# Performance work log

Hardware: AMD Instinct MI355X
Metric: run time of the kernel (lower is better)

## Reference

```python
import jax, jax.numpy as jnp
import numpy as np

B, N, IN_F, OUT_F = 8, 2048, 256, 256
ALPHA = 0.2  # LeakyReLU negative slope
NEG_INF = -1e9


def setup_inputs() -> dict:
    key = jax.random.key(0)
    ks = jax.random.split(key, 8)
    h = jax.random.normal(ks[0], (B, N, IN_F), dtype=jnp.float32)
    adj = jax.random.randint(ks[1], (B, N, N), 0, 2, dtype=jnp.int32)
    # xavier-ish scaled params
    W_w = jax.random.normal(ks[2], (OUT_F, IN_F), dtype=jnp.float32) * (1.414 / np.sqrt(IN_F + OUT_F))
    W_b = jnp.zeros((OUT_F,), dtype=jnp.float32)
    ai_w = jax.random.normal(ks[3], (1, OUT_F), dtype=jnp.float32) * (1.414 / np.sqrt(OUT_F + 1))
    ai_b = jnp.zeros((1,), dtype=jnp.float32)
    aj_w = jax.random.normal(ks[4], (1, OUT_F), dtype=jnp.float32) * (1.414 / np.sqrt(OUT_F + 1))
    aj_b = jnp.zeros((1,), dtype=jnp.float32)
    return {"h": h, "adj": adj, "W_w": W_w, "W_b": W_b,
            "ai_w": ai_w, "ai_b": ai_b, "aj_w": aj_w, "aj_b": aj_b}


def reference(h, adj, W_w, W_b, ai_w, ai_b, aj_w, aj_b):
    # Wh: [B, N, F]
    Wh = jnp.einsum('bni,oi->bno', h, W_w) + W_b
    # additive attention scores (pos_embed_dim == 1 so the .view is a transpose)
    Wh1 = jnp.einsum('bnf,of->bno', Wh, ai_w) + ai_b        # [B, N, 1]
    Wh2 = jnp.einsum('bnf,of->bno', Wh, aj_w) + aj_b        # [B, N, 1]
    e = Wh1 + jnp.swapaxes(Wh2, 1, 2)                       # [B, N, N]
    e = jnp.where(e >= 0, e, ALPHA * e)                     # LeakyReLU
    attention = jnp.where(adj > 0, e, NEG_INF)
    attention = jax.nn.softmax(attention, axis=2)
    # dropout: inference mode (training=False) -> identity
    h_hat = jnp.einsum('bnm,bmf->bnf', attention, Wh)
    return jax.nn.elu(h_hat)  # concat=True
```

## Files before the change

### kernel.cpp

```cpp
#include <hip/hip_runtime.h>

typedef __bf16 bf16;
typedef _Float16 f16;
typedef __bf16 bf16x8 __attribute__((ext_vector_type(8)));
typedef _Float16 f16x8 __attribute__((ext_vector_type(8)));
typedef float  f32x4  __attribute__((ext_vector_type(4)));

#define B_  8
#define N_  2048
#define F_  256
#define NTOK (B_ * N_)
#define NH   (NTOK * F_)
#define NW   (F_ * F_)
static constexpr float LOG2E = 1.44269504088896f;

__device__ __forceinline__ int detect_bf16(const void* h) {
    const unsigned* hw = (const unsigned*)h;
    unsigned w = hw[threadIdx.x & 63];
    unsigned ex = (w >> 7) & 0xFFu;
    unsigned long long b = __ballot(ex > 100u && ex < 150u);
    return __popcll(b) >= 40;
}

__device__ __forceinline__ float ldf(const void* p, int i, int isb) {
    return isb ? (float)((const bf16*)p)[i] : ((const float*)p)[i];
}

__device__ __forceinline__ size_t wht2_idx(int b, int f, int n) {
    int jc = n >> 6;
    int slot = ((n >> 3) & 7) ^ (f & 7);
    return (((size_t)(b * 32 + jc) * F_ + f) << 6) + (slot << 3) + (n & 7);
}

__global__ __launch_bounds__(256)
void k_cvt(const void* __restrict__ hv, const void* __restrict__ Wv,
           bf16* __restrict__ hb, bf16* __restrict__ Wb) {
    if (detect_bf16(hv)) return;
    size_t base = ((size_t)blockIdx.x * 256 + threadIdx.x) * 8;
    {
        const float* src = (const float*)hv + base;
        float4 a = *(const float4*)src;
        float4 b = *(const float4*)(src + 4);
        bf16x8 r;
        r[0]=(bf16)a.x; r[1]=(bf16)a.y; r[2]=(bf16)a.z; r[3]=(bf16)a.w;
        r[4]=(bf16)b.x; r[5]=(bf16)b.y; r[6]=(bf16)b.z; r[7]=(bf16)b.w;
        *(bf16x8*)(hb + base) = r;
    }
    if (base < NW) {
        const float* src = (const float*)Wv + base;
        float4 a = *(const float4*)src;
        float4 b = *(const float4*)(src + 4);
        bf16x8 r;
        r[0]=(bf16)a.x; r[1]=(bf16)a.y; r[2]=(bf16)a.z; r[3]=(bf16)a.w;
        r[4]=(bf16)b.x; r[5]=(bf16)b.y; r[6]=(bf16)b.z; r[7]=(bf16)b.w;
        *(bf16x8*)(Wb + base) = r;
    }
}

__global__ __launch_bounds__(256)
void k_wht(const void* __restrict__ hv, const void* __restrict__ Wv,
           const bf16* __restrict__ hcv, const bf16* __restrict__ Wcv,
           const void* __restrict__ Wbv, const void* __restrict__ ai_wv,
           const void* __restrict__ ai_bv, const void* __restrict__ aj_wv,
           const void* __restrict__ aj_bv, bf16* __restrict__ WhT2,
           unsigned* __restrict__ adjw) {
    int isb = detect_bf16(hv);
    const bf16* hb = isb ? (const bf16*)hv : hcv;
    const bf16* Wb = isb ? (const bf16*)Wv : Wcv;
    int ttile = blockIdx.x;
    int fg = threadIdx.x >> 6;
    int lane = threadIdx.x & 63;
    int T0 = ttile * 16;
    int m = lane & 15, quad = lane >> 4;

    f32x4 acc[4];
#pragma unroll
    for (int ft = 0; ft < 4; ++ft) acc[ft] = (f32x4){0.f, 0.f, 0.f, 0.f};

    const bf16* hp = hb + (size_t)(T0 + m) * F_ + quad * 8;
    const bf16* wp = Wb + (size_t)(fg * 64 + m) * F_ + quad * 8;
#pragma unroll
    for (int kk = 0; kk < F_; kk += 32) {
        bf16x8 hf = *(const bf16x8*)(hp + kk);
#pragma unroll
        for (int ft = 0; ft < 4; ++ft) {
            bf16x8 wf = *(const bf16x8*)(wp + (size_t)ft * 16 * F_ + kk);
            acc[ft] = __builtin_amdgcn_mfma_f32_16x16x32_bf16(wf, hf, acc[ft], 0, 0, 0);
        }
    }
    int token = T0 + m;
    int b = token >> 11, n = token & (N_ - 1);
    float s_p = 0.f, t_p = 0.f;
#pragma unroll
    for (int ft = 0; ft < 4; ++ft)
#pragma unroll
        for (int r = 0; r < 4; ++r) {
            int f = fg * 64 + ft * 16 + quad * 4 + r;
            float v = acc[ft][r] + ldf(Wbv, f, isb);
            bf16 vb = (bf16)v;
            WhT2[wht2_idx(b, f, n)] = vb;
            float vr = (float)vb;
            s_p += vr * ldf(ai_wv, f, isb);
            t_p += vr * ldf(aj_wv, f, isb);
        }
    s_p += __shfl_down(s_p, 32, 64); s_p += __shfl_down(s_p, 16, 64);
    t_p += __shfl_down(t_p, 32, 64); t_p += __shfl_down(t_p, 16, 64);
    __shared__ float sred[4][16], tred[4][16];
    if (lane < 16) { sred[fg][lane] = s_p; tred[fg][lane] = t_p; }
    __syncthreads();
    if (threadIdx.x < 16) {
        int tid = threadIdx.x;
        int tok = T0 + tid;
        float ss = (sred[0][tid] + sred[1][tid] + sred[2][tid] + sred[3][tid]
                    + ldf(ai_bv, 0, isb)) * LOG2E;
        float tt = (tred[0][tid] + tred[1][tid] + tred[2][tid] + tred[3][tid]
                    + ldf(aj_bv, 0, isb)) * LOG2E;
        f16 th = (f16)tt, sh = (f16)ss;
        unsigned short tu, su;
        __builtin_memcpy(&tu, &th, 2);
        __builtin_memcpy(&su, &sh, 2);
        unsigned w0 = adjw[tok];
        adjw[tok] = (w0 & 0xFFFFu) | ((unsigned)tu << 16);
        unsigned w1 = adjw[NTOK + tok];
        adjw[NTOK + tok] = (w1 & 0xFFFFu) | ((unsigned)su << 16);
    }
}

__device__ __forceinline__ unsigned char pbits(uint4 a, uint4 b) {
    return (unsigned char)((a.x & 1u) | ((a.y & 1u) << 1) | ((a.z & 1u) << 2) |
                           ((a.w & 1u) << 3) | ((b.x & 1u) << 4) |
                           ((b.y & 1u) << 5) | ((b.z & 1u) << 6) |
                           ((b.w & 1u) << 7));
}

__device__ __forceinline__ void stageB(const bf16* tile, char* dst,
                                       int w, int lane) {
#pragma unroll
    for (int r = 0; r < 8; ++r) {
        int off = (w * 8 + r) * 1024;
        const bf16* g = tile + off / 2 + lane * 8;
        __builtin_amdgcn_global_load_lds(
            (const __attribute__((address_space(1))) unsigned*)g,
            (__attribute__((address_space(3))) unsigned*)(dst + off),
            16, 0, 0);
    }
}

__global__ __launch_bounds__(256)
void k_attn(const unsigned* __restrict__ adjw, const bf16* __restrict__ WhT2,
            const void* __restrict__ hv, void* __restrict__ outv) {
    int isb = detect_bf16(hv);
    int bid = blockIdx.x;
    int b = bid & 7, itile = bid >> 3, i0 = itile * 32;
    int tid = threadIdx.x;
    int w = tid >> 6, lane = tid & 63, m = lane & 15, q = lane >> 4;
    int mt = w >> 1, jh = w & 1;

    __shared__ __align__(16) char smem[70656];
    char* Bbuf0 = smem;
    char* Bbuf1 = smem + 32768;
    f16* tLDS   = (f16*)(smem + 65536);
    unsigned char* pack0 = (unsigned char*)(smem + 69632);
    unsigned char* pack1 = (unsigned char*)(smem + 69888);
    float* red  = (float*)smem;

    const bf16* batch_tiles = WhT2 + ((size_t)b * 32) * F_ * 64;

#pragma unroll
    for (int k = 0; k < 8; ++k) {
        int idx = k * 256 + tid;
        unsigned wv = adjw[b * N_ + idx];
        unsigned short us = (unsigned short)(wv >> 16);
        f16 tv; __builtin_memcpy(&tv, &us, 2);
        tLDS[idx] = tv;
    }
    int row = i0 + mt * 16 + m;
    unsigned swd = adjw[NTOK + b * N_ + row];
    unsigned short su = (unsigned short)(swd >> 16);
    f16 sh; __builtin_memcpy(&sh, &su, 2);
    float s2i = (float)sh;

    int prow = tid >> 3, ps = tid & 7;
    const unsigned* arow = adjw + ((size_t)(b * N_ + i0 + prow)) * N_ + ps * 8;
    {
        uint4 x0 = *(const uint4*)arow, x1 = *(const uint4*)(arow + 4);
        pack0[prow * 8 + ps] = pbits(x0, x1);
    }
    stageB(batch_tiles, Bbuf0, w, lane);
    __syncthreads();

    bf16x8 ones;
#pragma unroll
    for (int k = 0; k < 8; ++k) ones[k] = (bf16)1.0f;

    f32x4 acc[16];
#pragma unroll
    for (int ft = 0; ft < 16; ++ft) acc[ft] = (f32x4){0.f, 0.f, 0.f, 0.f};
    f32x4 acc_l = {0.f, 0.f, 0.f, 0.f};

    for (int c = 0; c < 32; ++c) {
        char* Bcur = (c & 1) ? Bbuf1 : Bbuf0;
        unsigned char* pcur = (c & 1) ? pack1 : pack0;
        uint4 aw0, aw1;
        bool pre = (c < 31);
        if (pre) {
            stageB(batch_tiles + (size_t)(c + 1) * F_ * 64,
                   (c & 1) ? Bbuf0 : Bbuf1, w, lane);
            aw0 = *(const uint4*)(arow + (size_t)(c + 1) * 64);
            aw1 = *(const uint4*)(arow + (size_t)(c + 1) * 64 + 4);
        }
        unsigned long long pb64 =
            *(const unsigned long long*)(pcur + (mt * 16 + m) * 8);
        unsigned bits8 = (unsigned)(pb64 >> ((jh * 4 + q) * 8)) & 0xFFu;
        f16x8 tv = *(const f16x8*)(tLDS + c * 64 + jh * 32 + q * 8);

        bf16x8 af;
#pragma unroll
        for (int qq = 0; qq < 8; ++qq) {
            float x = s2i + (float)tv[qq];
            x = fmaxf(x, 0.2f * x);
            float pv = ((bits8 >> qq) & 1u) ? __builtin_amdgcn_exp2f(x) : 0.f;
            af[qq] = (bf16)pv;
        }
        int sbase = (jh * 4 + q);
#pragma unroll
        for (int ft = 0; ft < 16; ++ft) {
            int fr = ft * 16 + m;
            int psl = sbase ^ (m & 7);
            bf16x8 bfr = *(const bf16x8*)(Bcur + fr * 128 + psl * 16);
            acc[ft] = __builtin_amdgcn_mfma_f32_16x16x32_bf16(af, bfr, acc[ft], 0, 0, 0);
        }
        acc_l = __builtin_amdgcn_mfma_f32_16x16x32_bf16(af, ones, acc_l, 0, 0, 0);
        if (pre)
            ((c & 1) ? pack0 : pack1)[prow * 8 + ps] = pbits(aw0, aw1);
        __syncthreads();
    }

    if (jh == 1) {
#pragma unroll
        for (int r = 0; r < 4; ++r) {
            int rr = mt * 16 + q * 4 + r;
#pragma unroll
            for (int ft = 0; ft < 16; ++ft)
                red[rr * 257 + ft * 16 + m] = acc[ft][r];
            if (m == 0) red[rr * 257 + 256] = acc_l[r];
        }
    }
    __syncthreads();
    if (jh == 0) {
#pragma unroll
        for (int r = 0; r < 4; ++r) {
            int rr = mt * 16 + q * 4 + r;
            float lf = acc_l[r] + red[rr * 257 + 256];
            float rl = (lf > 0.f) ? (1.f / lf) : 0.f;
            size_t ob = ((size_t)b * N_ + i0 + rr) * F_;
#pragma unroll
            for (int ft = 0; ft < 16; ++ft) {
                int f = ft * 16 + m;
                float v = acc[ft][r] + red[rr * 257 + f];
                v *= rl;
                v = (v > 0.f) ? v : (__builtin_amdgcn_exp2f(v * LOG2E) - 1.f);
                if (isb) ((bf16*)outv)[ob + f] = (bf16)v;
                else     ((float*)outv)[ob + f] = v;
            }
        }
    }
}

extern "C" void kernel_launch(void* const* d_in, const int* in_sizes, int n_in,
                              void* d_out, int out_size, void* d_ws, size_t ws_size,
                              hipStream_t stream) {
    (void)in_sizes; (void)n_in; (void)out_size; (void)ws_size;
    const void* h    = d_in[0];
    unsigned*   adjw = (unsigned*)d_in[1];
    const void* W_w  = d_in[2];
    const void* W_b  = d_in[3];
    const void* ai_w = d_in[4];
    const void* ai_b = d_in[5];
    const void* aj_w = d_in[6];
    const void* aj_b = d_in[7];

    bf16* WhT2 = (bf16*)d_ws;
    bf16* hcv  = (bf16*)((char*)d_ws + (8  << 20));
    bf16* Wcv  = (bf16*)((char*)d_ws + (16 << 20));

    k_cvt <<<dim3(2048), dim3(256), 0, stream>>>(h, W_w, hcv, Wcv);
    k_wht <<<dim3(1024), dim3(256), 0, stream>>>(h, W_w, hcv, Wcv, W_b,
                                                 ai_w, ai_b, aj_w, aj_b,
                                                 WhT2, adjw);
    k_attn<<<dim3(512),  dim3(256), 0, stream>>>(adjw, WhT2, h, d_out);
}
```

Before: 262.4 us.

## Double attention row tile per block to reuse staged Wh fragments

Each block of the attention kernel now handles 64 query rows instead of 32. Each wave computes two 16-row MFMA tiles that share the same B-fragment LDS reads and the same staged Wh tiles. The grid is halved to 256 blocks and launch bounds are set to one block per CU, which allows larger accumulator register use. This cuts global and LDS traffic for Wh per output row. In exchange, fewer waves are resident per CU, so there is less latency hiding.

```diff
diff --git a/kernel.cpp b/kernel.cpp
--- a/kernel.cpp
+++ b/kernel.cpp
@@ -10,7 +10,6 @@
 #define N_  2048
 #define F_  256
 #define NTOK (B_ * N_)
-#define NH   (NTOK * F_)
 #define NW   (F_ * F_)
 static constexpr float LOG2E = 1.44269504088896f;
 
@@ -146,22 +145,22 @@
     }
 }
 
-__global__ __launch_bounds__(256)
+__global__ __launch_bounds__(256, 1)
 void k_attn(const unsigned* __restrict__ adjw, const bf16* __restrict__ WhT2,
             const void* __restrict__ hv, void* __restrict__ outv) {
     int isb = detect_bf16(hv);
     int bid = blockIdx.x;
-    int b = bid & 7, itile = bid >> 3, i0 = itile * 32;
+    int b = bid & 7, itile = bid >> 3, i0 = itile * 64;
     int tid = threadIdx.x;
     int w = tid >> 6, lane = tid & 63, m = lane & 15, q = lane >> 4;
-    int mt = w >> 1, jh = w & 1;
+    int mtq = w >> 1, jh = w & 1;
 
     __shared__ __align__(16) char smem[70656];
     char* Bbuf0 = smem;
     char* Bbuf1 = smem + 32768;
     f16* tLDS   = (f16*)(smem + 65536);
     unsigned char* pack0 = (unsigned char*)(smem + 69632);
-    unsigned char* pack1 = (unsigned char*)(smem + 69888);
+    unsigned char* pack1 = (unsigned char*)(smem + 70144);
     float* red  = (float*)smem;
 
     const bf16* batch_tiles = WhT2 + ((size_t)b * 32) * F_ * 64;
@@ -174,17 +173,25 @@
         f16 tv; __builtin_memcpy(&tv, &us, 2);
         tLDS[idx] = tv;
     }
-    int row = i0 + mt * 16 + m;
-    unsigned swd = adjw[NTOK + b * N_ + row];
-    unsigned short su = (unsigned short)(swd >> 16);
-    f16 sh; __builtin_memcpy(&sh, &su, 2);
-    float s2i = (float)sh;
-
-    int prow = tid >> 3, ps = tid & 7;
-    const unsigned* arow = adjw + ((size_t)(b * N_ + i0 + prow)) * N_ + ps * 8;
+    int row0 = i0 + mtq * 32 + m;
+    float s2i0, s2i1;
     {
-        uint4 x0 = *(const uint4*)arow, x1 = *(const uint4*)(arow + 4);
-        pack0[prow * 8 + ps] = pbits(x0, x1);
+        unsigned sw0 = adjw[NTOK + b * N_ + row0];
+        unsigned sw1 = adjw[NTOK + b * N_ + row0 + 16];
+        unsigned short u0 = (unsigned short)(sw0 >> 16);
+        unsigned short u1 = (unsigned short)(sw1 >> 16);
+        f16 h0, h1;
+        __builtin_memcpy(&h0, &u0, 2); __builtin_memcpy(&h1, &u1, 2);
+        s2i0 = (float)h0; s2i1 = (float)h1;
+    }
+
+    int pr = tid >> 2, pp = tid & 3;
+    const unsigned* arow = adjw + ((size_t)(b * N_ + i0 + pr)) * N_ + pp * 16;
+    {
+        uint4 x0 = *(const uint4*)arow,        x1 = *(const uint4*)(arow + 4);
+        uint4 x2 = *(const uint4*)(arow + 8),  x3 = *(const uint4*)(arow + 12);
+        pack0[pr * 8 + pp * 2]     = pbits(x0, x1);
+        pack0[pr * 8 + pp * 2 + 1] = pbits(x2, x3);
     }
     stageB(batch_tiles, Bbuf0, w, lane);
     __syncthreads();
@@ -193,34 +200,47 @@
 #pragma unroll
     for (int k = 0; k < 8; ++k) ones[k] = (bf16)1.0f;
 
-    f32x4 acc[16];
-#pragma unroll
-    for (int ft = 0; ft < 16; ++ft) acc[ft] = (f32x4){0.f, 0.f, 0.f, 0.f};
-    f32x4 acc_l = {0.f, 0.f, 0.f, 0.f};
+    f32x4 acc0[16], acc1[16];
+#pragma unroll
+    for (int ft = 0; ft < 16; ++ft) {
+        acc0[ft] = (f32x4){0.f, 0.f, 0.f, 0.f};
+        acc1[ft] = (f32x4){0.f, 0.f, 0.f, 0.f};
+    }
+    f32x4 acc_l0 = {0.f, 0.f, 0.f, 0.f};
+    f32x4 acc_l1 = {0.f, 0.f, 0.f, 0.f};
 
     for (int c = 0; c < 32; ++c) {
         char* Bcur = (c & 1) ? Bbuf1 : Bbuf0;
         unsigned char* pcur = (c & 1) ? pack1 : pack0;
-        uint4 aw0, aw1;
+        uint4 aw0, aw1, aw2, aw3;
         bool pre = (c < 31);
         if (pre) {
             stageB(batch_tiles + (size_t)(c + 1) * F_ * 64,
                    (c & 1) ? Bbuf0 : Bbuf1, w, lane);
-            aw0 = *(const uint4*)(arow + (size_t)(c + 1) * 64);
-            aw1 = *(const uint4*)(arow + (size_t)(c + 1) * 64 + 4);
-        }
-        unsigned long long pb64 =
-            *(const unsigned long long*)(pcur + (mt * 16 + m) * 8);
-        unsigned bits8 = (unsigned)(pb64 >> ((jh * 4 + q) * 8)) & 0xFFu;
+            const unsigned* ap = arow + (size_t)(c + 1) * 64;
+            aw0 = *(const uint4*)ap;       aw1 = *(const uint4*)(ap + 4);
+            aw2 = *(const uint4*)(ap + 8); aw3 = *(const uint4*)(ap + 12);
+        }
+        unsigned long long pb0 =
+            *(const unsigned long long*)(pcur + (mtq * 32 + m) * 8);
+        unsigned long long pb1 =
+            *(const unsigned long long*)(pcur + (mtq * 32 + 16 + m) * 8);
+        int sh8 = (jh * 4 + q) * 8;
+        unsigned bits0 = (unsigned)(pb0 >> sh8) & 0xFFu;
+        unsigned bits1 = (unsigned)(pb1 >> sh8) & 0xFFu;
         f16x8 tv = *(const f16x8*)(tLDS + c * 64 + jh * 32 + q * 8);
 
-        bf16x8 af;
+        bf16x8 af0, af1;
 #pragma unroll
         for (int qq = 0; qq < 8; ++qq) {
-            float x = s2i + (float)tv[qq];
-            x = fmaxf(x, 0.2f * x);
-            float pv = ((bits8 >> qq) & 1u) ? __builtin_amdgcn_exp2f(x) : 0.f;
-            af[qq] = (bf16)pv;
+            float tq = (float)tv[qq];
+            float x0 = s2i0 + tq, x1 = s2i1 + tq;
+            x0 = fmaxf(x0, 0.2f * x0);
+            x1 = fmaxf(x1, 0.2f * x1);
+            float p0 = ((bits0 >> qq) & 1u) ? __builtin_amdgcn_exp2f(x0) : 0.f;
+            float p1 = ((bits1 >> qq) & 1u) ? __builtin_amdgcn_exp2f(x1) : 0.f;
+            af0[qq] = (bf16)p0;
+            af1[qq] = (bf16)p1;
         }
         int sbase = (jh * 4 + q);
 #pragma unroll
@@ -228,36 +248,65 @@
             int fr = ft * 16 + m;
             int psl = sbase ^ (m & 7);
             bf16x8 bfr = *(const bf16x8*)(Bcur + fr * 128 + psl * 16);
-            acc[ft] = __builtin_amdgcn_mfma_f32_16x16x32_bf16(af, bfr, acc[ft], 0, 0, 0);
-        }
-        acc_l = __builtin_amdgcn_mfma_f32_16x16x32_bf16(af, ones, acc_l, 0, 0, 0);
-        if (pre)
-            ((c & 1) ? pack0 : pack1)[prow * 8 + ps] = pbits(aw0, aw1);
+            acc0[ft] = __builtin_amdgcn_mfma_f32_16x16x32_bf16(af0, bfr, acc0[ft], 0, 0, 0);
+            acc1[ft] = __builtin_amdgcn_mfma_f32_16x16x32_bf16(af1, bfr, acc1[ft], 0, 0, 0);
+        }
+        acc_l0 = __builtin_amdgcn_mfma_f32_16x16x32_bf16(af0, ones, acc_l0, 0, 0, 0);
+        acc_l1 = __builtin_amdgcn_mfma_f32_16x16x32_bf16(af1, ones, acc_l1, 0, 0, 0);
+        if (pre) {
+            unsigned char* pnxt = (c & 1) ? pack0 : pack1;
+            pnxt[pr * 8 + pp * 2]     = pbits(aw0, aw1);
+            pnxt[pr * 8 + pp * 2 + 1] = pbits(aw2, aw3);
+        }
         __syncthreads();
     }
 
     if (jh == 1) {
 #pragma unroll
         for (int r = 0; r < 4; ++r) {
-            int rr = mt * 16 + q * 4 + r;
+            int rr = mtq * 32 + q * 4 + r;
 #pragma unroll
             for (int ft = 0; ft < 16; ++ft)
-                red[rr * 257 + ft * 16 + m] = acc[ft][r];
-            if (m == 0) red[rr * 257 + 256] = acc_l[r];
+                red[rr * 257 + ft * 16 + m] = acc0[ft][r];
+            if (m == 0) red[rr * 257 + 256] = acc_l0[r];
+        }
+#pragma unroll
+        for (int r = 0; r < 4; ++r) {
+            int rr = mtq * 32 + 16 + q * 4 + r;
+#pragma unroll
+            for (int ft = 0; ft < 16; ++ft)
+                red[rr * 257 + ft * 16 + m] = acc1[ft][r];
+            if (m == 0) red[rr * 257 + 256] = acc_l1[r];
         }
     }
     __syncthreads();
     if (jh == 0) {
 #pragma unroll
         for (int r = 0; r < 4; ++r) {
-            int rr = mt * 16 + q * 4 + r;
-            float lf = acc_l[r] + red[rr * 257 + 256];
+            int rr = mtq * 32 + q * 4 + r;
+            float lf = acc_l0[r] + red[rr * 257 + 256];
             float rl = (lf > 0.f) ? (1.f / lf) : 0.f;
             size_t ob = ((size_t)b * N_ + i0 + rr) * F_;
 #pragma unroll
             for (int ft = 0; ft < 16; ++ft) {
                 int f = ft * 16 + m;
-                float v = acc[ft][r] + red[rr * 257 + f];
+                float v = acc0[ft][r] + red[rr * 257 + f];
+                v *= rl;
+                v = (v > 0.f) ? v : (__builtin_amdgcn_exp2f(v * LOG2E) - 1.f);
+                if (isb) ((bf16*)outv)[ob + f] = (bf16)v;
+                else     ((float*)outv)[ob + f] = v;
+            }
+        }
+#pragma unroll
+        for (int r = 0; r < 4; ++r) {
+            int rr = mtq * 32 + 16 + q * 4 + r;
+            float lf = acc_l1[r] + red[rr * 257 + 256];
+            float rl = (lf > 0.f) ? (1.f / lf) : 0.f;
+            size_t ob = ((size_t)b * N_ + i0 + rr) * F_;
+#pragma unroll
+            for (int ft = 0; ft < 16; ++ft) {
+                int f = ft * 16 + m;
+                float v = acc1[ft][r] + red[rr * 257 + f];
                 v *= rl;
                 v = (v > 0.f) ? v : (__builtin_amdgcn_exp2f(v * LOG2E) - 1.f);
                 if (isb) ((bf16*)outv)[ob + f] = (bf16)v;
@@ -288,5 +337,5 @@
     k_wht <<<dim3(1024), dim3(256), 0, stream>>>(h, W_w, hcv, Wcv, W_b,
                                                  ai_w, ai_b, aj_w, aj_b,
                                                  WhT2, adjw);
-    k_attn<<<dim3(512),  dim3(256), 0, stream>>>(adjw, WhT2, h, d_out);
-}
+    k_attn<<<dim3(256),  dim3(256), 0, stream>>>(adjw, WhT2, h, d_out);
+}
```

Result: slower. 275.4 us (+5.0%).

## Single-buffer attention B tiles for occupancy and stage WhT stores through LDS

Applied to the files above, without the earlier changes.

The attention kernel drops double buffering of the WhT tiles, cutting LDS from about 70KB to about 37KB and adding a launch-bounds hint of 4 blocks per CU to raise occupancy. Each chunk now loads its tile synchronously, then barriers before compute, so load/compute overlap within a block is lost and must be recovered by other resident blocks. Separately, the projection kernel stages its bf16 outputs in shared memory and writes 16-byte vectors to the swizzled WhT2 layout instead of scattered 2-byte stores.

```diff
diff --git a/kernel.cpp b/kernel.cpp
--- a/kernel.cpp
+++ b/kernel.cpp
@@ -10,7 +10,6 @@
 #define N_  2048
 #define F_  256
 #define NTOK (B_ * N_)
-#define NH   (NTOK * F_)
 #define NW   (F_ * F_)
 static constexpr float LOG2E = 1.44269504088896f;
 
@@ -26,11 +25,6 @@
     return isb ? (float)((const bf16*)p)[i] : ((const float*)p)[i];
 }
 
-__device__ __forceinline__ size_t wht2_idx(int b, int f, int n) {
-    int jc = n >> 6;
-    int slot = ((n >> 3) & 7) ^ (f & 7);
-    return (((size_t)(b * 32 + jc) * F_ + f) << 6) + (slot << 3) + (n & 7);
-}
 
 __global__ __launch_bounds__(256)
 void k_cvt(const void* __restrict__ hv, const void* __restrict__ Wv,
@@ -73,6 +67,9 @@
     int T0 = ttile * 16;
     int m = lane & 15, quad = lane >> 4;
 
+    __shared__ bf16 stage[F_ * 24];
+    __shared__ float sred[4][16], tred[4][16];
+
     f32x4 acc[4];
 #pragma unroll
     for (int ft = 0; ft < 4; ++ft) acc[ft] = (f32x4){0.f, 0.f, 0.f, 0.f};
@@ -88,8 +85,6 @@
             acc[ft] = __builtin_amdgcn_mfma_f32_16x16x32_bf16(wf, hf, acc[ft], 0, 0, 0);
         }
     }
-    int token = T0 + m;
-    int b = token >> 11, n = token & (N_ - 1);
     float s_p = 0.f, t_p = 0.f;
 #pragma unroll
     for (int ft = 0; ft < 4; ++ft)
@@ -98,16 +93,29 @@
             int f = fg * 64 + ft * 16 + quad * 4 + r;
             float v = acc[ft][r] + ldf(Wbv, f, isb);
             bf16 vb = (bf16)v;
-            WhT2[wht2_idx(b, f, n)] = vb;
+            stage[f * 24 + m] = vb;
             float vr = (float)vb;
             s_p += vr * ldf(ai_wv, f, isb);
             t_p += vr * ldf(aj_wv, f, isb);
         }
     s_p += __shfl_down(s_p, 32, 64); s_p += __shfl_down(s_p, 16, 64);
     t_p += __shfl_down(t_p, 32, 64); t_p += __shfl_down(t_p, 16, 64);
-    __shared__ float sred[4][16], tred[4][16];
     if (lane < 16) { sred[fg][lane] = s_p; tred[fg][lane] = t_p; }
     __syncthreads();
+
+    {
+        int f = threadIdx.x;
+        bf16x8 pk0 = *(const bf16x8*)(stage + f * 24);
+        bf16x8 pk1 = *(const bf16x8*)(stage + f * 24 + 8);
+        int b  = T0 >> 11;
+        int n0 = T0 & (N_ - 1);
+        int jc = n0 >> 6;
+        int s0 = (n0 >> 3) & 7;
+        char* rowp = (char*)WhT2 + ((size_t)(b * 32 + jc) * F_ + f) * 128;
+        *(bf16x8*)(rowp + (size_t)((s0)     ^ (f & 7)) * 16) = pk0;
+        *(bf16x8*)(rowp + (size_t)((s0 + 1) ^ (f & 7)) * 16) = pk1;
+    }
+
     if (threadIdx.x < 16) {
         int tid = threadIdx.x;
         int tok = T0 + tid;
@@ -146,7 +154,7 @@
     }
 }
 
-__global__ __launch_bounds__(256)
+__global__ __launch_bounds__(256, 4)
 void k_attn(const unsigned* __restrict__ adjw, const bf16* __restrict__ WhT2,
             const void* __restrict__ hv, void* __restrict__ outv) {
     int isb = detect_bf16(hv);
@@ -156,12 +164,11 @@
     int w = tid >> 6, lane = tid & 63, m = lane & 15, q = lane >> 4;
     int mt = w >> 1, jh = w & 1;
 
-    __shared__ __align__(16) char smem[70656];
-    char* Bbuf0 = smem;
-    char* Bbuf1 = smem + 32768;
-    f16* tLDS   = (f16*)(smem + 65536);
-    unsigned char* pack0 = (unsigned char*)(smem + 69632);
-    unsigned char* pack1 = (unsigned char*)(smem + 69888);
+    __shared__ __align__(16) char smem[37376];
+    char* Bbuf  = smem;
+    f16* tLDS   = (f16*)(smem + 32768);
+    unsigned char* pack0 = (unsigned char*)(smem + 36864);
+    unsigned char* pack1 = (unsigned char*)(smem + 37120);
     float* red  = (float*)smem;
 
     const bf16* batch_tiles = WhT2 + ((size_t)b * 32) * F_ * 64;
@@ -186,7 +193,6 @@
         uint4 x0 = *(const uint4*)arow, x1 = *(const uint4*)(arow + 4);
         pack0[prow * 8 + ps] = pbits(x0, x1);
     }
-    stageB(batch_tiles, Bbuf0, w, lane);
     __syncthreads();
 
     bf16x8 ones;
@@ -199,16 +205,16 @@
     f32x4 acc_l = {0.f, 0.f, 0.f, 0.f};
 
     for (int c = 0; c < 32; ++c) {
-        char* Bcur = (c & 1) ? Bbuf1 : Bbuf0;
         unsigned char* pcur = (c & 1) ? pack1 : pack0;
         uint4 aw0, aw1;
         bool pre = (c < 31);
+        stageB(batch_tiles + (size_t)c * F_ * 64, Bbuf, w, lane);
         if (pre) {
-            stageB(batch_tiles + (size_t)(c + 1) * F_ * 64,
-                   (c & 1) ? Bbuf0 : Bbuf1, w, lane);
             aw0 = *(const uint4*)(arow + (size_t)(c + 1) * 64);
             aw1 = *(const uint4*)(arow + (size_t)(c + 1) * 64 + 4);
         }
+        __syncthreads();
+
         unsigned long long pb64 =
             *(const unsigned long long*)(pcur + (mt * 16 + m) * 8);
         unsigned bits8 = (unsigned)(pb64 >> ((jh * 4 + q) * 8)) & 0xFFu;
@@ -227,7 +233,7 @@
         for (int ft = 0; ft < 16; ++ft) {
             int fr = ft * 16 + m;
             int psl = sbase ^ (m & 7);
-            bf16x8 bfr = *(const bf16x8*)(Bcur + fr * 128 + psl * 16);
+            bf16x8 bfr = *(const bf16x8*)(Bbuf + fr * 128 + psl * 16);
             acc[ft] = __builtin_amdgcn_mfma_f32_16x16x32_bf16(af, bfr, acc[ft], 0, 0, 0);
         }
         acc_l = __builtin_amdgcn_mfma_f32_16x16x32_bf16(af, ones, acc_l, 0, 0, 0);
```

After: 267.8 us. +2.1%, slower.
